# Performance work log

Hardware: AMD Instinct MI355X
Metric: run time of the kernel (lower is better)

The kernel has to match this reference:

```python
import jax, jax.numpy as jnp
import numpy as np

N = 100000   # nodes
E = 600000   # edges
G = 512      # graphs in batch
EPS = 1e-5   # LayerNorm eps
IN_DIM = 60 + 2 + 12  # dyn feats*frames + dims + st embedding
H = 128


def setup_inputs() -> dict:
    key = jax.random.key(0)
    ks = jax.random.split(key, 32)
    inp = {
        "x": jax.random.normal(ks[0], (N, 60), jnp.float32),
        "xdims": jax.random.uniform(ks[1], (N, 2), jnp.float32),
        "xsttype": jax.random.randint(ks[2], (N,), 0, 256, jnp.int32),
        "edge_index": jax.random.randint(ks[3], (2, E), 0, N, jnp.int32),
        "batch": jnp.sort(jax.random.randint(ks[4], (N,), 0, G, jnp.int32)),
        "emb": jax.random.normal(ks[5], (256, 12), jnp.float32),
    }
    def lin(k, i, o):
        s = 1.0 / np.sqrt(i)
        return jax.random.uniform(k, (i, o), jnp.float32, -s, s)
    dims = [IN_DIM, H, H]
    for l in range(2):
        i, o = dims[l], dims[l + 1]
        inp[f"Wl{l}"] = lin(ks[6 + 4 * l], i, o)   # lin_l: applied to aggregated neighbors
        inp[f"bl{l}"] = jnp.zeros((o,), jnp.float32)
        inp[f"Wr{l}"] = lin(ks[7 + 4 * l], i, o)   # lin_r: applied to root (no bias, PyG SAGEConv)
        inp[f"g{l}"] = jnp.ones((o,), jnp.float32)   # LayerNorm gamma
        inp[f"bn{l}"] = jnp.zeros((o,), jnp.float32)  # LayerNorm beta
    ld = [2 * H, 50, 50, 10]
    for l in range(3):
        inp[f"Wf{l}"] = lin(ks[20 + l], ld[l], ld[l + 1])
        inp[f"bf{l}"] = jnp.zeros((ld[l + 1],), jnp.float32)
    return inp


def _layer_norm(h, g, b):
    mu = jnp.mean(h, axis=-1, keepdims=True)
    var = jnp.mean(jnp.square(h - mu), axis=-1, keepdims=True)
    return (h - mu) * jax.lax.rsqrt(var + EPS) * g + b


def reference(x, xdims, xsttype, edge_index, batch, emb,
              Wl0, bl0, Wr0, g0, bn0,
              Wl1, bl1, Wr1, g1, bn1,
              Wf0, bf0, Wf1, bf1, Wf2, bf2):
    # node feature assembly: [N, 60+2+12]
    h = jnp.concatenate([x, xdims, emb[xsttype]], axis=1)

    src, dst = edge_index[0], edge_index[1]
    deg = jax.ops.segment_sum(jnp.ones((E,), h.dtype), dst, num_segments=N)
    inv_deg = (1.0 / jnp.maximum(deg, 1.0))[:, None]

    for Wl, bl, Wr, g, bn in ((Wl0, bl0, Wr0, g0, bn0), (Wl1, bl1, Wr1, g1, bn1)):
        # SAGEConv (mean aggr): out = lin_l(mean_j x_j) + lin_r(x_i)
        agg = jax.ops.segment_sum(h[src], dst, num_segments=N) * inv_deg
        h = agg @ Wl + bl + h @ Wr
        h = jax.nn.relu(_layer_norm(h, g, bn))  # dropout inactive (eval)

    # global mean / max pooling over graphs
    cnt = jax.ops.segment_sum(jnp.ones((N,), h.dtype), batch, num_segments=G)
    xmean = jax.ops.segment_sum(h, batch, num_segments=G) / jnp.maximum(cnt, 1.0)[:, None]
    xmax = jax.ops.segment_max(h, batch, num_segments=G)
    z = jnp.concatenate([xmean, xmax], axis=1)  # [G, 2H]

    for Wf, bf in ((Wf0, bf0), (Wf1, bf1), (Wf2, bf2)):
        z = jax.nn.relu(z @ Wf + bf)  # Linear + ReLU + Dropout(eval)
    return z
```

## Files before the change

kernel.cpp:

```cpp
#include <hip/hip_runtime.h>

#define NN 100000
#define NP 100096
#define EE 600000
#define GG 512
#define LN_EPS 1e-5f

typedef __attribute__((ext_vector_type(8))) __bf16 bf16x8;
typedef __attribute__((ext_vector_type(4))) float f32x4;

__device__ __forceinline__ unsigned short f2bf(float f) {
    unsigned int u = __float_as_uint(f);
    u = (u + 0x7fffu + ((u >> 16) & 1u)) >> 16;
    return (unsigned short)u;
}
__device__ __forceinline__ unsigned int pack2(float a, float b) {
    return (unsigned int)f2bf(a) | ((unsigned int)f2bf(b) << 16);
}
__device__ __forceinline__ void acc8(float* s, uint4 v) {
    s[0] += __uint_as_float(v.x << 16);
    s[1] += __uint_as_float(v.x & 0xffff0000u);
    s[2] += __uint_as_float(v.y << 16);
    s[3] += __uint_as_float(v.y & 0xffff0000u);
    s[4] += __uint_as_float(v.z << 16);
    s[5] += __uint_as_float(v.z & 0xffff0000u);
    s[6] += __uint_as_float(v.w << 16);
    s[7] += __uint_as_float(v.w & 0xffff0000u);
}

#define PREP_A (NP * 10)
#define PREP_W0 (128 * 160)
#define PREP_W1 (128 * 256)
#define PREP_TOT (PREP_A + PREP_W0 + PREP_W1 + EE)

__global__ __launch_bounds__(256) void prep_kernel(
    const float* __restrict__ x, const float* __restrict__ xdims,
    const int* __restrict__ stt, const float* __restrict__ emb,
    const int* __restrict__ ei,
    const float* __restrict__ Wl0, const float* __restrict__ Wr0,
    const float* __restrict__ Wl1, const float* __restrict__ Wr1,
    unsigned short* __restrict__ H0r,
    unsigned short* __restrict__ Wt0, unsigned short* __restrict__ Wt1,
    int* __restrict__ deg)
{
    int idx = blockIdx.x * 256 + threadIdx.x;
    if (idx < PREP_A) {
        int node = idx / 10;
        int c8 = (idx - node * 10) * 8;
        unsigned short vals[8];
        if (node < NN) {
            int st = stt[node];
            #pragma unroll
            for (int i = 0; i < 8; ++i) {
                int f = c8 + i;
                float v = 0.f;
                if (f < 60)      v = x[node * 60 + f];
                else if (f < 62) v = xdims[node * 2 + (f - 60)];
                else if (f < 74) v = emb[st * 12 + (f - 62)];
                vals[i] = f2bf(v);
            }
        } else {
            #pragma unroll
            for (int i = 0; i < 8; ++i) vals[i] = 0;
        }
        uint4 o;
        o.x = (unsigned)vals[0] | ((unsigned)vals[1] << 16);
        o.y = (unsigned)vals[2] | ((unsigned)vals[3] << 16);
        o.z = (unsigned)vals[4] | ((unsigned)vals[5] << 16);
        o.w = (unsigned)vals[6] | ((unsigned)vals[7] << 16);
        *(uint4*)(H0r + (size_t)node * 80 + c8) = o;
    } else if (idx < PREP_A + PREP_W0) {
        int j = idx - PREP_A;
        int n = j / 160, k = j - n * 160;
        float v = 0.f;
        if (k < 74)                  v = Wl0[k * 128 + n];
        else if (k >= 80 && k < 154) v = Wr0[(k - 80) * 128 + n];
        Wt0[(size_t)n * 160 + k] = f2bf(v);
    } else if (idx < PREP_A + PREP_W0 + PREP_W1) {
        int j = idx - PREP_A - PREP_W0;
        int n = j >> 8, k = j & 255;
        float v = (k < 128) ? Wl1[k * 128 + n] : Wr1[(k - 128) * 128 + n];
        Wt1[(size_t)n * 256 + k] = f2bf(v);
    } else if (idx < PREP_TOT) {
        int e = idx - PREP_A - PREP_W0 - PREP_W1;
        atomicAdd(&deg[ei[EE + e]], 1);
    }
}

__global__ __launch_bounds__(256) void scan1_kernel(
    const int* __restrict__ deg, int* __restrict__ offs, int* __restrict__ bsum)
{
    __shared__ int ts[256];
    int t = threadIdx.x;
    int base = blockIdx.x * 2048 + t * 8;
    int d[8];
    if (base + 8 <= NN) {
        int4 a = *(const int4*)&deg[base];
        int4 b = *(const int4*)&deg[base + 4];
        d[0]=a.x; d[1]=a.y; d[2]=a.z; d[3]=a.w;
        d[4]=b.x; d[5]=b.y; d[6]=b.z; d[7]=b.w;
    } else {
        #pragma unroll
        for (int i = 0; i < 8; ++i) d[i] = (base + i < NN) ? deg[base + i] : 0;
    }
    int e[8]; int run = 0;
    #pragma unroll
    for (int i = 0; i < 8; ++i) { e[i] = run; run += d[i]; }
    ts[t] = run;
    int tot = run;
    __syncthreads();
    for (int off = 1; off < 256; off <<= 1) {
        int u = (t >= off) ? ts[t - off] : 0;
        __syncthreads();
        ts[t] += u;
        __syncthreads();
    }
    int pre = ts[t] - tot;
    #pragma unroll
    for (int i = 0; i < 8; ++i) if (base + i < NN) offs[base + i] = e[i] + pre;
    if (t == 255) bsum[blockIdx.x] = ts[255];
}

__global__ void scan2_kernel(int* __restrict__ bsum, int nb)
{
    int t = threadIdx.x;
    int v = (t < nb) ? bsum[t] : 0;
    int inc = v;
    for (int off = 1; off < 64; off <<= 1) {
        int u = __shfl_up(inc, off, 64);
        if (t >= off) inc += u;
    }
    if (t < nb) bsum[t] = inc - v;
}

__global__ __launch_bounds__(256) void fill_csr_kernel(
    const int* __restrict__ ei, int* __restrict__ cur,
    const int* __restrict__ offs, const int* __restrict__ bsum,
    int* __restrict__ csr)
{
    int e = blockIdx.x * 256 + threadIdx.x;
    if (e >= EE) return;
    int d = ei[EE + e];
    int p = offs[d] + bsum[d >> 11] + atomicAdd(&cur[d], 1);
    csr[p] = ei[e];
}

__global__ __launch_bounds__(256) void agg0_kernel(
    const unsigned short* __restrict__ H0r, unsigned short* __restrict__ A0g,
    const int* __restrict__ csr, const int* __restrict__ offs,
    const int* __restrict__ bsum, const int* __restrict__ deg)
{
    int node = blockIdx.x * 16 + (threadIdx.x >> 4);
    int lane = threadIdx.x & 15;
    if (node >= NP || lane >= 10) return;
    int d = 0, st = 0;
    if (node < NN) { d = deg[node]; st = offs[node] + bsum[node >> 11]; }
    float iv = 1.0f / (float)(d > 1 ? d : 1);
    float s[8];
    #pragma unroll
    for (int i = 0; i < 8; ++i) s[i] = 0.f;
    int e = 0;
    for (; e + 4 <= d; e += 4) {
        int i0 = csr[st + e],     i1 = csr[st + e + 1];
        int i2 = csr[st + e + 2], i3 = csr[st + e + 3];
        uint4 v0 = *(const uint4*)(H0r + (size_t)i0 * 80 + lane * 8);
        uint4 v1 = *(const uint4*)(H0r + (size_t)i1 * 80 + lane * 8);
        uint4 v2 = *(const uint4*)(H0r + (size_t)i2 * 80 + lane * 8);
        uint4 v3 = *(const uint4*)(H0r + (size_t)i3 * 80 + lane * 8);
        acc8(s, v0); acc8(s, v1); acc8(s, v2); acc8(s, v3);
    }
    for (; e < d; ++e) {
        int i0 = csr[st + e];
        uint4 v0 = *(const uint4*)(H0r + (size_t)i0 * 80 + lane * 8);
        acc8(s, v0);
    }
    uint4 o;
    o.x = pack2(s[0] * iv, s[1] * iv);
    o.y = pack2(s[2] * iv, s[3] * iv);
    o.z = pack2(s[4] * iv, s[5] * iv);
    o.w = pack2(s[6] * iv, s[7] * iv);
    *(uint4*)(A0g + (size_t)node * 80 + lane * 8) = o;
}

__global__ __launch_bounds__(256) void agg1_kernel(
    const unsigned short* __restrict__ H1, unsigned short* __restrict__ A1g,
    const int* __restrict__ csr, const int* __restrict__ offs,
    const int* __restrict__ bsum, const int* __restrict__ deg)
{
    int node = blockIdx.x * 16 + (threadIdx.x >> 4);
    int lane = threadIdx.x & 15;
    if (node >= NP) return;
    int d = 0, st = 0;
    if (node < NN) { d = deg[node]; st = offs[node] + bsum[node >> 11]; }
    float iv = 1.0f / (float)(d > 1 ? d : 1);
    float s[8];
    #pragma unroll
    for (int i = 0; i < 8; ++i) s[i] = 0.f;
    int e = 0;
    for (; e + 4 <= d; e += 4) {
        int i0 = csr[st + e],     i1 = csr[st + e + 1];
        int i2 = csr[st + e + 2], i3 = csr[st + e + 3];
        uint4 v0 = *(const uint4*)(H1 + (size_t)i0 * 128 + lane * 8);
        uint4 v1 = *(const uint4*)(H1 + (size_t)i1 * 128 + lane * 8);
        uint4 v2 = *(const uint4*)(H1 + (size_t)i2 * 128 + lane * 8);
        uint4 v3 = *(const uint4*)(H1 + (size_t)i3 * 128 + lane * 8);
        acc8(s, v0); acc8(s, v1); acc8(s, v2); acc8(s, v3);
    }
    for (; e < d; ++e) {
        int i0 = csr[st + e];
        uint4 v0 = *(const uint4*)(H1 + (size_t)i0 * 128 + lane * 8);
        acc8(s, v0);
    }
    uint4 o;
    o.x = pack2(s[0] * iv, s[1] * iv);
    o.y = pack2(s[2] * iv, s[3] * iv);
    o.z = pack2(s[4] * iv, s[5] * iv);
    o.w = pack2(s[6] * iv, s[7] * iv);
    *(uint4*)(A1g + (size_t)node * 128 + lane * 8) = o;
}

template<int K, bool POOL>
__global__ __launch_bounds__(256, 4) void gemm_kernel(
    const unsigned short* __restrict__ Ag,
    const unsigned short* __restrict__ Hr,
    const unsigned short* __restrict__ Wt,
    const float* __restrict__ bias, const float* __restrict__ gamma,
    const float* __restrict__ beta,
    unsigned short* __restrict__ outH,
    const int* __restrict__ batch,
    float* __restrict__ psum, int* __restrict__ pmax)
{
    constexpr int KT = K / 32, AS = K + 8, CPR = K / 8, CPRh = CPR / 2, KH = K / 2;
    constexpr int ASMB = 64 * AS * 2;
    constexpr int SMEM = (!POOL || ASMB > 64 * 128 * 4) ? ASMB : 64 * 128 * 4;
    __shared__ __align__(16) char smem[SMEM];
    unsigned short* Asm = (unsigned short*)smem;
    float* Hs = (float*)smem;
    __shared__ __align__(16) float sP[64 * 4];
    __shared__ __align__(16) float qP[64 * 4];
    __shared__ int bS[POOL ? 64 : 1];

    const int tid = threadIdx.x;
    const int n0 = blockIdx.x * 64;

    if (POOL && tid < 64) {
        int gn = n0 + tid;
        bS[tid] = (gn < NN) ? batch[gn] : -1;
    }
    for (int i = tid; i < 64 * CPR; i += 256) {
        int node = i / CPR, c = i - node * CPR;
        size_t gn = (size_t)(n0 + node);
        const unsigned short* src = (c < CPRh)
            ? (Ag + gn * KH + c * 8)
            : (Hr + gn * KH + (c - CPRh) * 8);
        uint4 v = *(const uint4*)src;
        *(uint4*)(Asm + node * AS + c * 8) = v;
    }

    const int l = tid & 63, w = tid >> 6;
    const int g = l >> 4, c0 = l & 15;
    float bia[2], gam[2], bet[2];
    #pragma unroll
    for (int j = 0; j < 2; ++j) {
        int col = (2 * w + j) * 16 + c0;
        bia[j] = bias[col]; gam[j] = gamma[col]; bet[j] = beta[col];
    }
    const unsigned short* bp0 = Wt + (size_t)((2 * w + 0) * 16 + c0) * K + g * 8;
    const unsigned short* bp1 = Wt + (size_t)((2 * w + 1) * 16 + c0) * K + g * 8;
    const unsigned short* ar = Asm + c0 * AS + g * 8;
    __syncthreads();

    f32x4 acc[4][2];
    #pragma unroll
    for (int m = 0; m < 4; ++m) {
        acc[m][0] = (f32x4){0.f,0.f,0.f,0.f};
        acc[m][1] = (f32x4){0.f,0.f,0.f,0.f};
    }

    #pragma unroll
    for (int kt = 0; kt < KT; ++kt) {
        bf16x8 b0 = *(const bf16x8*)(bp0 + kt * 32);
        bf16x8 b1 = *(const bf16x8*)(bp1 + kt * 32);
        bf16x8 a0 = *(const bf16x8*)(ar + 0 * 16 * AS + kt * 32);
        bf16x8 a1 = *(const bf16x8*)(ar + 1 * 16 * AS + kt * 32);
        bf16x8 a2 = *(const bf16x8*)(ar + 2 * 16 * AS + kt * 32);
        bf16x8 a3 = *(const bf16x8*)(ar + 3 * 16 * AS + kt * 32);
        acc[0][0] = __builtin_amdgcn_mfma_f32_16x16x32_bf16(a0, b0, acc[0][0], 0, 0, 0);
        acc[0][1] = __builtin_amdgcn_mfma_f32_16x16x32_bf16(a0, b1, acc[0][1], 0, 0, 0);
        acc[1][0] = __builtin_amdgcn_mfma_f32_16x16x32_bf16(a1, b0, acc[1][0], 0, 0, 0);
        acc[1][1] = __builtin_amdgcn_mfma_f32_16x16x32_bf16(a1, b1, acc[1][1], 0, 0, 0);
        acc[2][0] = __builtin_amdgcn_mfma_f32_16x16x32_bf16(a2, b0, acc[2][0], 0, 0, 0);
        acc[2][1] = __builtin_amdgcn_mfma_f32_16x16x32_bf16(a2, b1, acc[2][1], 0, 0, 0);
        acc[3][0] = __builtin_amdgcn_mfma_f32_16x16x32_bf16(a3, b0, acc[3][0], 0, 0, 0);
        acc[3][1] = __builtin_amdgcn_mfma_f32_16x16x32_bf16(a3, b1, acc[3][1], 0, 0, 0);
    }

    #pragma unroll
    for (int m = 0; m < 4; ++m) {
        #pragma unroll
        for (int r = 0; r < 4; ++r) {
            float h0v = acc[m][0][r] + bia[0];
            float h1v = acc[m][1][r] + bia[1];
            float s = h0v + h1v, q = h0v * h0v + h1v * h1v;
            #pragma unroll
            for (int mm = 1; mm < 16; mm <<= 1) {
                s += __shfl_xor(s, mm, 64);
                q += __shfl_xor(q, mm, 64);
            }
            if (c0 == 0) {
                int node = m * 16 + g * 4 + r;
                sP[node * 4 + w] = s;
                qP[node * 4 + w] = q;
            }
        }
    }
    __syncthreads();

    #pragma unroll
    for (int m = 0; m < 4; ++m) {
        #pragma unroll
        for (int r = 0; r < 4; ++r) {
            int node = m * 16 + g * 4 + r;
            float4 sv = *(const float4*)&sP[node * 4];
            float4 qv = *(const float4*)&qP[node * 4];
            float s = (sv.x + sv.y) + (sv.z + sv.w);
            float q = (qv.x + qv.y) + (qv.z + qv.w);
            float mu   = s * (1.f / 128.f);
            float var  = q * (1.f / 128.f) - mu * mu;
            float rinv = rsqrtf(var + LN_EPS);
            float h0v = acc[m][0][r] + bia[0];
            float h1v = acc[m][1][r] + bia[1];
            float v0 = fmaxf(0.f, (h0v - mu) * rinv * gam[0] + bet[0]);
            float v1 = fmaxf(0.f, (h1v - mu) * rinv * gam[1] + bet[1]);
            if (POOL) {
                Hs[node * 128 + (2 * w) * 16 + c0]     = v0;
                Hs[node * 128 + (2 * w + 1) * 16 + c0] = v1;
            } else {
                size_t gn = (size_t)(n0 + node);
                outH[gn * 128 + (2 * w) * 16 + c0]     = f2bf(v0);
                outH[gn * 128 + (2 * w + 1) * 16 + c0] = f2bf(v1);
            }
        }
    }
    if (!POOL) return;
    __syncthreads();

    if (tid < 128) {
        int j = tid;
        int curg = -1; float s = 0.f, m = 0.f;
        #pragma unroll 4
        for (int n = 0; n < 64; ++n) {
            int gb = bS[n];
            if (gb < 0) break;
            if (gb != curg) {
                if (curg >= 0) {
                    atomicAdd(&psum[curg * 128 + j], s);
                    atomicMax(&pmax[curg * 128 + j], __float_as_int(m));
                }
                curg = gb; s = 0.f; m = 0.f;
            }
            float v = Hs[n * 128 + j];
            s += v; m = fmaxf(m, v);
        }
        if (curg >= 0) {
            atomicAdd(&psum[curg * 128 + j], s);
            atomicMax(&pmax[curg * 128 + j], __float_as_int(m));
        }
    }
}

__device__ __forceinline__ int lbound(const int* a, int n, int v) {
    int lo = 0, hi = n;
    while (lo < hi) { int mid = (lo + hi) >> 1; if (a[mid] < v) lo = mid + 1; else hi = mid; }
    return lo;
}

__global__ __launch_bounds__(64) void mlp_kernel(
    const float* __restrict__ psum, const int* __restrict__ pmax,
    const int* __restrict__ batch,
    const float* __restrict__ Wf0, const float* __restrict__ bf0,
    const float* __restrict__ Wf1, const float* __restrict__ bf1,
    const float* __restrict__ Wf2, const float* __restrict__ bf2,
    float* __restrict__ out)
{
    __shared__ float z[256];
    __shared__ float t1[50];
    __shared__ float t2[50];
    __shared__ int cS;
    int g = blockIdx.x, t = threadIdx.x;
    if (t == 0) cS = lbound(batch, NN, g + 1) - lbound(batch, NN, g);
    __syncthreads();
    int c = cS;
    float ic = 1.0f / (float)(c > 1 ? c : 1);
    for (int j = t; j < 128; j += 64) {
        z[j]       = psum[g * 128 + j] * ic;
        z[128 + j] = __int_as_float(pmax[g * 128 + j]);
    }
    __syncthreads();
    if (t < 50) {
        float a = bf0[t];
        for (int k = 0; k < 256; ++k) a = fmaf(z[k], Wf0[k * 50 + t], a);
        t1[t] = fmaxf(a, 0.0f);
    }
    __syncthreads();
    if (t < 50) {
        float a = bf1[t];
        for (int k = 0; k < 50; ++k) a = fmaf(t1[k], Wf1[k * 50 + t], a);
        t2[t] = fmaxf(a, 0.0f);
    }
    __syncthreads();
    if (t < 10) {
        float a = bf2[t];
        for (int k = 0; k < 50; ++k) a = fmaf(t2[k], Wf2[k * 10 + t], a);
        out[g * 10 + t] = fmaxf(a, 0.0f);
    }
}

extern "C" void kernel_launch(void* const* d_in, const int* in_sizes, int n_in,
                              void* d_out, int out_size, void* d_ws, size_t ws_size,
                              hipStream_t stream)
{
    const float* x     = (const float*)d_in[0];
    const float* xdims = (const float*)d_in[1];
    const int*   stt   = (const int*)d_in[2];
    const int*   ei    = (const int*)d_in[3];
    const int*   batch = (const int*)d_in[4];
    const float* emb   = (const float*)d_in[5];
    const float* Wl0   = (const float*)d_in[6];
    const float* bl0   = (const float*)d_in[7];
    const float* Wr0   = (const float*)d_in[8];
    const float* g0    = (const float*)d_in[9];
    const float* bn0   = (const float*)d_in[10];
    const float* Wl1   = (const float*)d_in[11];
    const float* bl1   = (const float*)d_in[12];
    const float* Wr1   = (const float*)d_in[13];
    const float* g1    = (const float*)d_in[14];
    const float* bn1   = (const float*)d_in[15];
    const float* Wf0   = (const float*)d_in[16];
    const float* bf0   = (const float*)d_in[17];
    const float* Wf1   = (const float*)d_in[18];
    const float* bf1   = (const float*)d_in[19];
    const float* Wf2   = (const float*)d_in[20];
    const float* bf2   = (const float*)d_in[21];

    char* w = (char*)d_ws;
    unsigned short* H0r = (unsigned short*)w; w += (size_t)NP * 80 * 2;
    unsigned short* A0g = (unsigned short*)w; w += (size_t)NP * 80 * 2;
    unsigned short* H1  = (unsigned short*)w; w += (size_t)NP * 128 * 2;
    unsigned short* A1g = (unsigned short*)w; w += (size_t)NP * 128 * 2;
    unsigned short* Wt0 = (unsigned short*)w; w += (size_t)128 * 160 * 2;
    unsigned short* Wt1 = (unsigned short*)w; w += (size_t)128 * 256 * 2;
    int*   csr    = (int*)w;   w += (size_t)EE * 4;
    int*   offs   = (int*)w;   w += (size_t)NN * 4;
    int*   bsum   = (int*)w;   w += 1024;
    char* zbeg = w;
    int*   deg  = (int*)w;   w += (size_t)NP * 4;
    int*   cur  = (int*)w;   w += (size_t)NN * 4;
    float* psum = (float*)w; w += (size_t)GG * 128 * 4;
    int*   pmax = (int*)w;   w += (size_t)GG * 128 * 4;
    size_t zsz = (size_t)(w - zbeg);

    hipMemsetAsync(zbeg, 0, zsz, stream);

    prep_kernel<<<(PREP_TOT + 255) / 256, 256, 0, stream>>>(
        x, xdims, stt, emb, ei, Wl0, Wr0, Wl1, Wr1, H0r, Wt0, Wt1, deg);

    int nb = (NN + 2047) / 2048;
    scan1_kernel<<<nb, 256, 0, stream>>>(deg, offs, bsum);
    scan2_kernel<<<1, 64, 0, stream>>>(bsum, nb);
    fill_csr_kernel<<<(EE + 255) / 256, 256, 0, stream>>>(ei, cur, offs, bsum, csr);

    agg0_kernel<<<NP / 16, 256, 0, stream>>>(H0r, A0g, csr, offs, bsum, deg);
    gemm_kernel<160, false><<<NP / 64, 256, 0, stream>>>(
        A0g, H0r, Wt0, bl0, g0, bn0, H1, nullptr, nullptr, nullptr);
    agg1_kernel<<<NP / 16, 256, 0, stream>>>(H1, A1g, csr, offs, bsum, deg);
    gemm_kernel<256, true><<<NP / 64, 256, 0, stream>>>(
        A1g, H1, Wt1, bl1, g1, bn1, nullptr, batch, psum, pmax);

    mlp_kernel<<<GG, 64, 0, stream>>>(psum, pmax, batch, Wf0, bf0, Wf1, bf1, Wf2, bf2,
                                      (float*)d_out);
}
```

Baseline: 318.3 us.

## Split GEMM node tile into two halves and prefetch second half during first

The 64-node A tile in the SAGE GEMM kernel is now staged as two 32-node halves. The first half goes to shared memory as before. The second half is loaded into registers and written to a separate shared buffer only after the first half's MFMA loop has run. This is meant to hide global-load latency of half the tile behind matrix work. The cost is extra live registers (a prefetch array sized by K) under launch bounds of 4 blocks per CU, plus one additional block barrier.

```diff
diff --git a/kernel.cpp b/kernel.cpp
--- a/kernel.cpp
+++ b/kernel.cpp
@@ -231,10 +231,13 @@
     float* __restrict__ psum, int* __restrict__ pmax)
 {
     constexpr int KT = K / 32, AS = K + 8, CPR = K / 8, CPRh = CPR / 2, KH = K / 2;
-    constexpr int ASMB = 64 * AS * 2;
+    constexpr int BUF = 32 * AS;
+    constexpr int NPRE = (32 * CPR + 255) / 256;
+    constexpr int ASMB = 2 * BUF * 2;
     constexpr int SMEM = (!POOL || ASMB > 64 * 128 * 4) ? ASMB : 64 * 128 * 4;
     __shared__ __align__(16) char smem[SMEM];
-    unsigned short* Asm = (unsigned short*)smem;
+    unsigned short* A0s = (unsigned short*)smem;
+    unsigned short* A1s = A0s + BUF;
     float* Hs = (float*)smem;
     __shared__ __align__(16) float sP[64 * 4];
     __shared__ __align__(16) float qP[64 * 4];
@@ -247,14 +250,26 @@
         int gn = n0 + tid;
         bS[tid] = (gn < NN) ? batch[gn] : -1;
     }
-    for (int i = tid; i < 64 * CPR; i += 256) {
+    for (int i = tid; i < 32 * CPR; i += 256) {
         int node = i / CPR, c = i - node * CPR;
         size_t gn = (size_t)(n0 + node);
         const unsigned short* src = (c < CPRh)
             ? (Ag + gn * KH + c * 8)
             : (Hr + gn * KH + (c - CPRh) * 8);
-        uint4 v = *(const uint4*)src;
-        *(uint4*)(Asm + node * AS + c * 8) = v;
+        *(uint4*)(A0s + node * AS + c * 8) = *(const uint4*)src;
+    }
+    uint4 pre[NPRE];
+    #pragma unroll
+    for (int p = 0; p < NPRE; ++p) {
+        int i = tid + p * 256;
+        if (i < 32 * CPR) {
+            int node = i / CPR, c = i - node * CPR;
+            size_t gn = (size_t)(n0 + 32 + node);
+            const unsigned short* src = (c < CPRh)
+                ? (Ag + gn * KH + c * 8)
+                : (Hr + gn * KH + (c - CPRh) * 8);
+            pre[p] = *(const uint4*)src;
+        }
     }
 
     const int l = tid & 63, w = tid >> 6;
@@ -267,78 +282,107 @@
     }
     const unsigned short* bp0 = Wt + (size_t)((2 * w + 0) * 16 + c0) * K + g * 8;
     const unsigned short* bp1 = Wt + (size_t)((2 * w + 1) * 16 + c0) * K + g * 8;
-    const unsigned short* ar = Asm + c0 * AS + g * 8;
-    __syncthreads();
-
-    f32x4 acc[4][2];
-    #pragma unroll
-    for (int m = 0; m < 4; ++m) {
-        acc[m][0] = (f32x4){0.f,0.f,0.f,0.f};
-        acc[m][1] = (f32x4){0.f,0.f,0.f,0.f};
-    }
-
-    #pragma unroll
-    for (int kt = 0; kt < KT; ++kt) {
-        bf16x8 b0 = *(const bf16x8*)(bp0 + kt * 32);
-        bf16x8 b1 = *(const bf16x8*)(bp1 + kt * 32);
-        bf16x8 a0 = *(const bf16x8*)(ar + 0 * 16 * AS + kt * 32);
-        bf16x8 a1 = *(const bf16x8*)(ar + 1 * 16 * AS + kt * 32);
-        bf16x8 a2 = *(const bf16x8*)(ar + 2 * 16 * AS + kt * 32);
-        bf16x8 a3 = *(const bf16x8*)(ar + 3 * 16 * AS + kt * 32);
-        acc[0][0] = __builtin_amdgcn_mfma_f32_16x16x32_bf16(a0, b0, acc[0][0], 0, 0, 0);
-        acc[0][1] = __builtin_amdgcn_mfma_f32_16x16x32_bf16(a0, b1, acc[0][1], 0, 0, 0);
-        acc[1][0] = __builtin_amdgcn_mfma_f32_16x16x32_bf16(a1, b0, acc[1][0], 0, 0, 0);
-        acc[1][1] = __builtin_amdgcn_mfma_f32_16x16x32_bf16(a1, b1, acc[1][1], 0, 0, 0);
-        acc[2][0] = __builtin_amdgcn_mfma_f32_16x16x32_bf16(a2, b0, acc[2][0], 0, 0, 0);
-        acc[2][1] = __builtin_amdgcn_mfma_f32_16x16x32_bf16(a2, b1, acc[2][1], 0, 0, 0);
-        acc[3][0] = __builtin_amdgcn_mfma_f32_16x16x32_bf16(a3, b0, acc[3][0], 0, 0, 0);
-        acc[3][1] = __builtin_amdgcn_mfma_f32_16x16x32_bf16(a3, b1, acc[3][1], 0, 0, 0);
-    }
-
-    #pragma unroll
-    for (int m = 0; m < 4; ++m) {
+    __syncthreads();
+
+    f32x4 acc[2][2][2];
+    #pragma unroll
+    for (int t = 0; t < 2; ++t)
         #pragma unroll
-        for (int r = 0; r < 4; ++r) {
-            float h0v = acc[m][0][r] + bia[0];
-            float h1v = acc[m][1][r] + bia[1];
-            float s = h0v + h1v, q = h0v * h0v + h1v * h1v;
+        for (int m = 0; m < 2; ++m) {
+            acc[t][m][0] = (f32x4){0.f,0.f,0.f,0.f};
+            acc[t][m][1] = (f32x4){0.f,0.f,0.f,0.f};
+        }
+
+    {
+        const unsigned short* ar0 = A0s + (0 * 16 + c0) * AS + g * 8;
+        const unsigned short* ar1 = A0s + (1 * 16 + c0) * AS + g * 8;
+        #pragma unroll
+        for (int kt = 0; kt < KT; ++kt) {
+            bf16x8 b0 = *(const bf16x8*)(bp0 + kt * 32);
+            bf16x8 b1 = *(const bf16x8*)(bp1 + kt * 32);
+            bf16x8 a0 = *(const bf16x8*)(ar0 + kt * 32);
+            bf16x8 a1 = *(const bf16x8*)(ar1 + kt * 32);
+            acc[0][0][0] = __builtin_amdgcn_mfma_f32_16x16x32_bf16(a0, b0, acc[0][0][0], 0, 0, 0);
+            acc[0][0][1] = __builtin_amdgcn_mfma_f32_16x16x32_bf16(a0, b1, acc[0][0][1], 0, 0, 0);
+            acc[0][1][0] = __builtin_amdgcn_mfma_f32_16x16x32_bf16(a1, b0, acc[0][1][0], 0, 0, 0);
+            acc[0][1][1] = __builtin_amdgcn_mfma_f32_16x16x32_bf16(a1, b1, acc[0][1][1], 0, 0, 0);
+        }
+    }
+    #pragma unroll
+    for (int p = 0; p < NPRE; ++p) {
+        int i = tid + p * 256;
+        if (i < 32 * CPR) {
+            int node = i / CPR, c = i - node * CPR;
+            *(uint4*)(A1s + node * AS + c * 8) = pre[p];
+        }
+    }
+    __syncthreads();
+    {
+        const unsigned short* ar0 = A1s + (0 * 16 + c0) * AS + g * 8;
+        const unsigned short* ar1 = A1s + (1 * 16 + c0) * AS + g * 8;
+        #pragma unroll
+        for (int kt = 0; kt < KT; ++kt) {
+            bf16x8 b0 = *(const bf16x8*)(bp0 + kt * 32);
+            bf16x8 b1 = *(const bf16x8*)(bp1 + kt * 32);
+            bf16x8 a0 = *(const bf16x8*)(ar0 + kt * 32);
+            bf16x8 a1 = *(const bf16x8*)(ar1 + kt * 32);
+            acc[1][0][0] = __builtin_amdgcn_mfma_f32_16x16x32_bf16(a0, b0, acc[1][0][0], 0, 0, 0);
+            acc[1][0][1] = __builtin_amdgcn_mfma_f32_16x16x32_bf16(a0, b1, acc[1][0][1], 0, 0, 0);
+            acc[1][1][0] = __builtin_amdgcn_mfma_f32_16x16x32_bf16(a1, b0, acc[1][1][0], 0, 0, 0);
+            acc[1][1][1] = __builtin_amdgcn_mfma_f32_16x16x32_bf16(a1, b1, acc[1][1][1], 0, 0, 0);
+        }
+    }
+
+    #pragma unroll
+    for (int t = 0; t < 2; ++t) {
+        #pragma unroll
+        for (int m = 0; m < 2; ++m) {
             #pragma unroll
-            for (int mm = 1; mm < 16; mm <<= 1) {
-                s += __shfl_xor(s, mm, 64);
-                q += __shfl_xor(q, mm, 64);
+            for (int r = 0; r < 4; ++r) {
+                float h0v = acc[t][m][0][r] + bia[0];
+                float h1v = acc[t][m][1][r] + bia[1];
+                float s = h0v + h1v, q = h0v * h0v + h1v * h1v;
+                #pragma unroll
+                for (int mm = 1; mm < 16; mm <<= 1) {
+                    s += __shfl_xor(s, mm, 64);
+                    q += __shfl_xor(q, mm, 64);
+                }
+                if (c0 == 0) {
+                    int node = t * 32 + m * 16 + g * 4 + r;
+                    sP[node * 4 + w] = s;
+                    qP[node * 4 + w] = q;
+                }
             }
-            if (c0 == 0) {
-                int node = m * 16 + g * 4 + r;
-                sP[node * 4 + w] = s;
-                qP[node * 4 + w] = q;
-            }
-        }
-    }
-    __syncthreads();
-
-    #pragma unroll
-    for (int m = 0; m < 4; ++m) {
+        }
+    }
+    __syncthreads();
+
+    #pragma unroll
+    for (int t = 0; t < 2; ++t) {
         #pragma unroll
-        for (int r = 0; r < 4; ++r) {
-            int node = m * 16 + g * 4 + r;
-            float4 sv = *(const float4*)&sP[node * 4];
-            float4 qv = *(const float4*)&qP[node * 4];
-            float s = (sv.x + sv.y) + (sv.z + sv.w);
-            float q = (qv.x + qv.y) + (qv.z + qv.w);
-            float mu   = s * (1.f / 128.f);
-            float var  = q * (1.f / 128.f) - mu * mu;
-            float rinv = rsqrtf(var + LN_EPS);
-            float h0v = acc[m][0][r] + bia[0];
-            float h1v = acc[m][1][r] + bia[1];
-            float v0 = fmaxf(0.f, (h0v - mu) * rinv * gam[0] + bet[0]);
-            float v1 = fmaxf(0.f, (h1v - mu) * rinv * gam[1] + bet[1]);
-            if (POOL) {
-                Hs[node * 128 + (2 * w) * 16 + c0]     = v0;
-                Hs[node * 128 + (2 * w + 1) * 16 + c0] = v1;
-            } else {
-                size_t gn = (size_t)(n0 + node);
-                outH[gn * 128 + (2 * w) * 16 + c0]     = f2bf(v0);
-                outH[gn * 128 + (2 * w + 1) * 16 + c0] = f2bf(v1);
+        for (int m = 0; m < 2; ++m) {
+            #pragma unroll
+            for (int r = 0; r < 4; ++r) {
+                int node = t * 32 + m * 16 + g * 4 + r;
+                float4 sv = *(const float4*)&sP[node * 4];
+                float4 qv = *(const float4*)&qP[node * 4];
+                float s = (sv.x + sv.y) + (sv.z + sv.w);
+                float q = (qv.x + qv.y) + (qv.z + qv.w);
+                float mu   = s * (1.f / 128.f);
+                float var  = q * (1.f / 128.f) - mu * mu;
+                float rinv = rsqrtf(var + LN_EPS);
+                float h0v = acc[t][m][0][r] + bia[0];
+                float h1v = acc[t][m][1][r] + bia[1];
+                float v0 = fmaxf(0.f, (h0v - mu) * rinv * gam[0] + bet[0]);
+                float v1 = fmaxf(0.f, (h1v - mu) * rinv * gam[1] + bet[1]);
+                if (POOL) {
+                    Hs[node * 128 + (2 * w) * 16 + c0]     = v0;
+                    Hs[node * 128 + (2 * w + 1) * 16 + c0] = v1;
+                } else {
+                    size_t gn = (size_t)(n0 + node);
+                    outH[gn * 128 + (2 * w) * 16 + c0]     = f2bf(v0);
+                    outH[gn * 128 + (2 * w + 1) * 16 + c0] = f2bf(v1);
+                }
             }
         }
     }
```

Measured after the change: 328.3 us. 3.1% more time.
